# Kernel optimization log

Measured on AMD Instinct MI355X. Metric: run time of the kernel, lower is better.

The kernel has to match this reference:

```python
import jax, jax.numpy as jnp
import numpy as np

B, S_NEW, DIM = 32, 1, 4096
H, KV, HD = 32, 8, 128          # query heads, kv heads, head_dim
PREV = 2048                      # tokens already in the KV cache


def setup_inputs() -> dict:
    key = jax.random.key(0)
    ks = jax.random.split(key, 8)
    return {
        "x": jax.random.normal(ks[0], (B, S_NEW, DIM), jnp.float32),
        "wq": jax.random.normal(ks[1], (DIM, H * HD), jnp.float32) * 0.02,
        "wk": jax.random.normal(ks[2], (DIM, KV * HD), jnp.float32) * 0.02,
        "wv": jax.random.normal(ks[3], (DIM, KV * HD), jnp.float32) * 0.02,
        "wo": jax.random.normal(ks[4], (H * HD, DIM), jnp.float32) * 0.02,
        "cache_k": jax.random.normal(ks[5], (B, PREV, KV, HD), jnp.float32),
        "cache_v": jax.random.normal(ks[6], (B, PREV, KV, HD), jnp.float32),
        "freqs": jax.random.normal(ks[7], (S_NEW, HD // 2), jnp.float32),  # rotary angles (angle of freqs_cis)
    }


def _apply_rope(t, cos, sin):
    # t: [b, s, h, hd]; interleaved pairs as in torch.view_as_complex
    a = t[..., 0::2]
    b = t[..., 1::2]
    c = cos[None, :, None, :]
    s = sin[None, :, None, :]
    ra = a * c - b * s
    rb = a * s + b * c
    return jnp.stack([ra, rb], axis=-1).reshape(t.shape)


def reference(x, wq, wk, wv, wo, cache_k, cache_v, freqs):
    b, s, _ = x.shape  # s == 1 (decode)
    xq = (x @ wq).reshape(b, s, H, HD)
    xk = (x @ wk).reshape(b, s, KV, HD)
    xv = (x @ wv).reshape(b, s, KV, HD)

    cos, sin = jnp.cos(freqs), jnp.sin(freqs)
    xq = _apply_rope(xq, cos, sin)
    xk = _apply_rope(xk, cos, sin)

    # KV-cache append (update_cache_decode)
    k_full = jnp.concatenate([cache_k, xk], axis=1)  # [b, PREV+1, KV, hd]
    v_full = jnp.concatenate([cache_v, xv], axis=1)

    # GQA attention without materializing the expanded cache
    g = H // KV
    q = xq.reshape(b, KV, g, HD)  # s == 1 folded away
    scale = 1.0 / jnp.sqrt(jnp.asarray(HD, x.dtype))
    scores = jnp.einsum("bkgd,bskd->bkgs", q, k_full) * scale  # [b, KV, g, PREV+1]
    attn = jax.nn.softmax(scores, axis=-1)
    out = jnp.einsum("bkgs,bskd->bkgd", attn, v_full)  # [b, KV, g, hd]
    out = out.reshape(b, s, H * HD)
    return out @ wo
```

## Files before the change

kernel.cpp:

```cpp
#include <hip/hip_runtime.h>


#define WS_P1   0
#define WS_QKV  6291456
#define WS_ATTN 6488064
#define WS_P2   6619136

__global__ __launch_bounds__(256) void gemm_skinny(
    const float* __restrict__ X,
    const float* __restrict__ W0, int e0, int ld0,
    const float* __restrict__ W1, int e1, int ld1,
    const float* __restrict__ W2, int ld2,
    float* __restrict__ P, int Ntot)
{
    __shared__ float x_t[128][36];
    __shared__ float2 red[128][33];

    const int nb = blockIdx.x * 256;
    const float* W; int ld, noff;
    if (nb < e0)      { W = W0; ld = ld0; noff = 0;  }
    else if (nb < e1) { W = W1; ld = ld1; noff = e0; }
    else              { W = W2; ld = ld2; noff = e1; }

    const int k0  = blockIdx.y * 128;
    const int tid = threadIdx.x;
    const int cp  = tid & 127;
    const int kg  = tid >> 7;
    const int nn  = nb - noff + cp * 2;

    #pragma unroll
    for (int i = 0; i < 16; ++i) {
        int idx = tid + i * 256;
        int bb = idx >> 7, kk = idx & 127;
        x_t[kk][bb] = X[(size_t)bb * 4096 + k0 + kk];
    }
    __syncthreads();

    float2 acc[32];
    #pragma unroll
    for (int b = 0; b < 32; ++b) { acc[b].x = 0.f; acc[b].y = 0.f; }

    const float* Wp = W + (size_t)k0 * ld + nn;
    for (int kk0 = kg * 64; kk0 < kg * 64 + 64; kk0 += 8) {
        float2 w[8];
        #pragma unroll
        for (int u = 0; u < 8; ++u)
            w[u] = *(const float2*)&Wp[(size_t)(kk0 + u) * ld];
        #pragma unroll
        for (int u = 0; u < 8; ++u) {
            const float* xr = x_t[kk0 + u];
            #pragma unroll
            for (int bq = 0; bq < 8; ++bq) {
                float4 xv = *(const float4*)&xr[bq * 4];
                acc[bq*4+0].x += xv.x * w[u].x; acc[bq*4+0].y += xv.x * w[u].y;
                acc[bq*4+1].x += xv.y * w[u].x; acc[bq*4+1].y += xv.y * w[u].y;
                acc[bq*4+2].x += xv.z * w[u].x; acc[bq*4+2].y += xv.z * w[u].y;
                acc[bq*4+3].x += xv.w * w[u].x; acc[bq*4+3].y += xv.w * w[u].y;
            }
        }
    }

    if (kg == 1) {
        #pragma unroll
        for (int b = 0; b < 32; ++b) red[cp][b] = acc[b];
    }
    __syncthreads();
    if (kg == 0) {
        const int ks = blockIdx.y;
        #pragma unroll
        for (int b = 0; b < 32; ++b) {
            float2 o = red[cp][b];
            float2 v; v.x = acc[b].x + o.x; v.y = acc[b].y + o.y;
            *(float2*)&P[((size_t)ks * 32 + b) * Ntot + nb + cp * 2] = v;
        }
    }
}

__global__ __launch_bounds__(256) void reduce_rope(
    const float* __restrict__ P, const float* __restrict__ freqs,
    float* __restrict__ qkv)
{
    int t = blockIdx.x * 256 + threadIdx.x;
    int b = t / 3072;
    int cp = t - b * 3072;
    int n = cp * 2;
    float sx = 0.f, sy = 0.f;
    #pragma unroll
    for (int ks = 0; ks < 32; ++ks) {
        float2 v = *(const float2*)&P[((size_t)ks * 32 + b) * 6144 + n];
        sx += v.x; sy += v.y;
    }
    if (n < 5120) {
        int d = n & 127;
        float fr = freqs[d >> 1];
        float c = cosf(fr), s = sinf(fr);
        float ra = sx * c - sy * s;
        float rb = sx * s + sy * c;
        if (n < 4096) {
            const float sc = 0.08838834764831845f;
            ra *= sc; rb *= sc;
        }
        sx = ra; sy = rb;
    }
    float2 o; o.x = sx; o.y = sy;
    *(float2*)&qkv[(size_t)b * 6144 + n] = o;
}

__global__ __launch_bounds__(1024) void attn_kernel(
    const float* __restrict__ qkv,
    const float* __restrict__ ck, const float* __restrict__ cv,
    float* __restrict__ ao)
{
    __shared__ float sbuf[8208];
    __shared__ float red[4][4];
    __shared__ float mxv[4];
    __shared__ float inv[4];

    const int b  = blockIdx.x >> 3;
    const int kv = blockIdx.x & 7;
    const int tid = threadIdx.x;
    const int wave = tid >> 6, lane = tid & 63;
    const int psub = (lane >> 4) & 3, dl = lane & 15;

    float q[4][8];
    {
        const float* qb = qkv + (size_t)b * 6144 + kv * 512 + dl * 8;
        #pragma unroll
        for (int h = 0; h < 4; ++h) {
            float4 a = *(const float4*)&qb[h * 128];
            float4 c = *(const float4*)&qb[h * 128 + 4];
            q[h][0]=a.x; q[h][1]=a.y; q[h][2]=a.z; q[h][3]=a.w;
            q[h][4]=c.x; q[h][5]=c.y; q[h][6]=c.z; q[h][7]=c.w;
        }
    }

    if (tid < 16) {
        const float* kr = qkv + (size_t)b * 6144 + 4096 + kv * 128 + dl * 8;
        float4 k0 = *(const float4*)kr;
        float4 k1 = *(const float4*)(kr + 4);
        float p[4];
        #pragma unroll
        for (int h = 0; h < 4; ++h) {
            p[h] = q[h][0]*k0.x + q[h][1]*k0.y + q[h][2]*k0.z + q[h][3]*k0.w
                 + q[h][4]*k1.x + q[h][5]*k1.y + q[h][6]*k1.z + q[h][7]*k1.w;
        }
        #pragma unroll
        for (int off = 1; off < 16; off <<= 1) {
            #pragma unroll
            for (int h = 0; h < 4; ++h) p[h] += __shfl_xor(p[h], off);
        }
        if (dl == 0) {
            #pragma unroll
            for (int h = 0; h < 4; ++h) sbuf[h * 2052 + 2048] = p[h];
        }
    }

    const float* kbase = ck + ((size_t)b * 2048 * 8 + kv) * 128;
    const int srow = wave * 4 + psub;
    for (int it0 = 0; it0 < 32; it0 += 4) {
        float4 kA[4][2];
        #pragma unroll
        for (int u = 0; u < 4; ++u) {
            const float* kr = kbase + (size_t)((it0 + u) * 64 + srow) * 1024 + dl * 8;
            kA[u][0] = *(const float4*)kr;
            kA[u][1] = *(const float4*)(kr + 4);
        }
        #pragma unroll
        for (int u = 0; u < 4; ++u) {
            int s = (it0 + u) * 64 + srow;
            float p[4];
            #pragma unroll
            for (int h = 0; h < 4; ++h) {
                p[h] = q[h][0]*kA[u][0].x + q[h][1]*kA[u][0].y
                     + q[h][2]*kA[u][0].z + q[h][3]*kA[u][0].w
                     + q[h][4]*kA[u][1].x + q[h][5]*kA[u][1].y
                     + q[h][6]*kA[u][1].z + q[h][7]*kA[u][1].w;
            }
            #pragma unroll
            for (int off = 1; off < 16; off <<= 1) {
                #pragma unroll
                for (int h = 0; h < 4; ++h) p[h] += __shfl_xor(p[h], off);
            }
            if (dl == 0) {
                #pragma unroll
                for (int h = 0; h < 4; ++h) sbuf[h * 2052 + s] = p[h];
            }
        }
    }
    __syncthreads();

    const int h = tid >> 8, r = tid & 255;
    float m = -1e30f;
    for (int s = r; s < 2049; s += 256) m = fmaxf(m, sbuf[h * 2052 + s]);
    #pragma unroll
    for (int off = 1; off < 64; off <<= 1) m = fmaxf(m, __shfl_xor(m, off));
    if (lane == 0) red[h][wave & 3] = m;
    __syncthreads();
    if (r == 0)
        mxv[h] = fmaxf(fmaxf(red[h][0], red[h][1]), fmaxf(red[h][2], red[h][3]));
    __syncthreads();
    const float mx = mxv[h];
    float sum = 0.f;
    for (int s = r; s < 2049; s += 256) {
        float p = __expf(sbuf[h * 2052 + s] - mx);
        sbuf[h * 2052 + s] = p;
        sum += p;
    }
    #pragma unroll
    for (int off = 1; off < 64; off <<= 1) sum += __shfl_xor(sum, off);
    if (lane == 0) red[h][wave & 3] = sum;
    __syncthreads();
    if (r == 0) inv[h] = 1.0f / (red[h][0] + red[h][1] + red[h][2] + red[h][3]);
    __syncthreads();

    const int grp = tid >> 5, l32 = tid & 31, d4 = l32 * 4;
    float4 acc[4];
    #pragma unroll
    for (int hh = 0; hh < 4; ++hh) { acc[hh].x=0.f; acc[hh].y=0.f; acc[hh].z=0.f; acc[hh].w=0.f; }
    const float* vbase = cv + ((size_t)b * 2048 * 8 + kv) * 128;
    for (int it = 0; it < 16; ++it) {
        float4 vv[4];
        float pp[4][4];
        #pragma unroll
        for (int j = 0; j < 4; ++j) {
            int s = it * 128 + j * 32 + grp;
            vv[j] = *(const float4*)&vbase[(size_t)s * 1024 + d4];
        }
        #pragma unroll
        for (int j = 0; j < 4; ++j) {
            int s = it * 128 + j * 32 + grp;
            #pragma unroll
            for (int hh = 0; hh < 4; ++hh) pp[j][hh] = sbuf[hh * 2052 + s];
        }
        #pragma unroll
        for (int j = 0; j < 4; ++j) {
            #pragma unroll
            for (int hh = 0; hh < 4; ++hh) {
                acc[hh].x += pp[j][hh] * vv[j].x;
                acc[hh].y += pp[j][hh] * vv[j].y;
                acc[hh].z += pp[j][hh] * vv[j].z;
                acc[hh].w += pp[j][hh] * vv[j].w;
            }
        }
    }
    if (grp == 0) {
        const float* vr = qkv + (size_t)b * 6144 + 5120 + kv * 128;
        float4 v = *(const float4*)&vr[d4];
        #pragma unroll
        for (int hh = 0; hh < 4; ++hh) {
            float p = sbuf[hh * 2052 + 2048];
            acc[hh].x += p * v.x; acc[hh].y += p * v.y;
            acc[hh].z += p * v.z; acc[hh].w += p * v.w;
        }
    }
    __syncthreads();

    #pragma unroll
    for (int hh = 0; hh < 4; ++hh) {
        acc[hh].x += __shfl_down(acc[hh].x, 32);
        acc[hh].y += __shfl_down(acc[hh].y, 32);
        acc[hh].z += __shfl_down(acc[hh].z, 32);
        acc[hh].w += __shfl_down(acc[hh].w, 32);
    }
    if (lane < 32) {
        #pragma unroll
        for (int hh = 0; hh < 4; ++hh)
            *(float4*)&sbuf[wave * 512 + hh * 128 + d4] = acc[hh];
    }
    __syncthreads();

    if (tid < 512) {
        int hh = tid >> 7, d = tid & 127;
        float v = 0.f;
        #pragma unroll
        for (int w = 0; w < 16; ++w) v += sbuf[w * 512 + hh * 128 + d];
        ao[(size_t)b * 4096 + kv * 512 + hh * 128 + d] = v * inv[hh];
    }
}

__global__ __launch_bounds__(256) void reduce_out(
    const float* __restrict__ P, float* __restrict__ out)
{
    int t = blockIdx.x * 256 + threadIdx.x;
    int b = t >> 11;
    int cp = t & 2047;
    int n = cp * 2;
    float sx = 0.f, sy = 0.f;
    #pragma unroll
    for (int ks = 0; ks < 32; ++ks) {
        float2 v = *(const float2*)&P[((size_t)ks * 32 + b) * 4096 + n];
        sx += v.x; sy += v.y;
    }
    float2 o; o.x = sx; o.y = sy;
    *(float2*)&out[(size_t)b * 4096 + n] = o;
}

extern "C" void kernel_launch(void* const* d_in, const int* in_sizes, int n_in,
                              void* d_out, int out_size, void* d_ws, size_t ws_size,
                              hipStream_t stream) {
    const float* x  = (const float*)d_in[0];
    const float* wq = (const float*)d_in[1];
    const float* wk = (const float*)d_in[2];
    const float* wv = (const float*)d_in[3];
    const float* wo = (const float*)d_in[4];
    const float* ck = (const float*)d_in[5];
    const float* cv = (const float*)d_in[6];
    const float* fr = (const float*)d_in[7];
    float* out = (float*)d_out;
    float* ws  = (float*)d_ws;

    float* P1   = ws + WS_P1;
    float* qkv  = ws + WS_QKV;
    float* attn = ws + WS_ATTN;
    float* P2   = ws + WS_P2;

    dim3 g1(24, 32);
    gemm_skinny<<<g1, 256, 0, stream>>>(x, wq, 4096, 4096, wk, 5120, 1024,
                                        wv, 1024, P1, 6144);
    reduce_rope<<<384, 256, 0, stream>>>(P1, fr, qkv);
    attn_kernel<<<256, 1024, 0, stream>>>(qkv, ck, cv, attn);
    dim3 g4(16, 32);
    gemm_skinny<<<g4, 256, 0, stream>>>(attn, wo, 4096, 4096, wo, 4096, 4096,
                                        wo, 4096, P2, 4096);
    reduce_out<<<256, 256, 0, stream>>>(P2, out);
}
```

Baseline: 183.7 us.

## Split attention over sequence chunks with flash-decoding style combine kernel

Replaces the single 1024-thread attention block per (batch, kv-head) with four 256-thread blocks, each covering a 512-token slice of the KV cache. Each block writes its partial max, sum and unnormalized output to a workspace, and a new combine kernel merges them with log-sum-exp rescaling. This raises the block count from 256 to 1024, so more CUs get work and more memory requests are in flight while streaming the cache. The cost is an extra kernel launch and a small workspace round-trip.

```diff
diff --git a/kernel.cpp b/kernel.cpp
--- a/kernel.cpp
+++ b/kernel.cpp
@@ -5,6 +5,7 @@
 #define WS_QKV  6291456
 #define WS_ATTN 6488064
 #define WS_P2   6619136
+#define WS_PA   10813440
 
 __global__ __launch_bounds__(256) void gemm_skinny(
     const float* __restrict__ X,
@@ -106,21 +107,22 @@
     *(float2*)&qkv[(size_t)b * 6144 + n] = o;
 }
 
-__global__ __launch_bounds__(1024) void attn_kernel(
+__global__ __launch_bounds__(256, 4) void attn_split(
     const float* __restrict__ qkv,
     const float* __restrict__ ck, const float* __restrict__ cv,
-    float* __restrict__ ao)
-{
-    __shared__ float sbuf[8208];
-    __shared__ float red[4][4];
-    __shared__ float mxv[4];
-    __shared__ float inv[4];
-
-    const int b  = blockIdx.x >> 3;
-    const int kv = blockIdx.x & 7;
+    float* __restrict__ pa)
+{
+    __shared__ float sbuf[4096];
+    __shared__ float pm[4], pl[4];
+
+    const int blk = blockIdx.x;
+    const int c   = blk & 3;
+    const int kv  = (blk >> 2) & 7;
+    const int b   = blk >> 5;
     const int tid = threadIdx.x;
     const int wave = tid >> 6, lane = tid & 63;
     const int psub = (lane >> 4) & 3, dl = lane & 15;
+    const int s0 = c * 512;
 
     float q[4][8];
     {
@@ -128,13 +130,13 @@
         #pragma unroll
         for (int h = 0; h < 4; ++h) {
             float4 a = *(const float4*)&qb[h * 128];
-            float4 c = *(const float4*)&qb[h * 128 + 4];
+            float4 e = *(const float4*)&qb[h * 128 + 4];
             q[h][0]=a.x; q[h][1]=a.y; q[h][2]=a.z; q[h][3]=a.w;
-            q[h][4]=c.x; q[h][5]=c.y; q[h][6]=c.z; q[h][7]=c.w;
-        }
-    }
-
-    if (tid < 16) {
+            q[h][4]=e.x; q[h][5]=e.y; q[h][6]=e.z; q[h][7]=e.w;
+        }
+    }
+
+    if (c == 3 && tid < 16) {
         const float* kr = qkv + (size_t)b * 6144 + 4096 + kv * 128 + dl * 8;
         float4 k0 = *(const float4*)kr;
         float4 k1 = *(const float4*)(kr + 4);
@@ -151,23 +153,24 @@
         }
         if (dl == 0) {
             #pragma unroll
-            for (int h = 0; h < 4; ++h) sbuf[h * 2052 + 2048] = p[h];
-        }
-    }
-
-    const float* kbase = ck + ((size_t)b * 2048 * 8 + kv) * 128;
+            for (int h = 0; h < 4; ++h) sbuf[h * 520 + 512] = p[h];
+        }
+    }
+
+    const float* kbase = ck + ((size_t)b * 2048 * 8 + kv) * 128
+                            + (size_t)s0 * 1024;
     const int srow = wave * 4 + psub;
     for (int it0 = 0; it0 < 32; it0 += 4) {
         float4 kA[4][2];
         #pragma unroll
         for (int u = 0; u < 4; ++u) {
-            const float* kr = kbase + (size_t)((it0 + u) * 64 + srow) * 1024 + dl * 8;
+            const float* kr = kbase + (size_t)((it0 + u) * 16 + srow) * 1024 + dl * 8;
             kA[u][0] = *(const float4*)kr;
             kA[u][1] = *(const float4*)(kr + 4);
         }
         #pragma unroll
         for (int u = 0; u < 4; ++u) {
-            int s = (it0 + u) * 64 + srow;
+            int s = (it0 + u) * 16 + srow;
             float p[4];
             #pragma unroll
             for (int h = 0; h < 4; ++h) {
@@ -183,54 +186,50 @@
             }
             if (dl == 0) {
                 #pragma unroll
-                for (int h = 0; h < 4; ++h) sbuf[h * 2052 + s] = p[h];
-            }
-        }
-    }
-    __syncthreads();
-
-    const int h = tid >> 8, r = tid & 255;
-    float m = -1e30f;
-    for (int s = r; s < 2049; s += 256) m = fmaxf(m, sbuf[h * 2052 + s]);
-    #pragma unroll
-    for (int off = 1; off < 64; off <<= 1) m = fmaxf(m, __shfl_xor(m, off));
-    if (lane == 0) red[h][wave & 3] = m;
-    __syncthreads();
-    if (r == 0)
-        mxv[h] = fmaxf(fmaxf(red[h][0], red[h][1]), fmaxf(red[h][2], red[h][3]));
-    __syncthreads();
-    const float mx = mxv[h];
-    float sum = 0.f;
-    for (int s = r; s < 2049; s += 256) {
-        float p = __expf(sbuf[h * 2052 + s] - mx);
-        sbuf[h * 2052 + s] = p;
-        sum += p;
-    }
-    #pragma unroll
-    for (int off = 1; off < 64; off <<= 1) sum += __shfl_xor(sum, off);
-    if (lane == 0) red[h][wave & 3] = sum;
-    __syncthreads();
-    if (r == 0) inv[h] = 1.0f / (red[h][0] + red[h][1] + red[h][2] + red[h][3]);
+                for (int h = 0; h < 4; ++h) sbuf[h * 520 + s] = p[h];
+            }
+        }
+    }
+    __syncthreads();
+
+    {
+        const int h = wave;
+        const int nrow = (c == 3) ? 513 : 512;
+        float m = -1e30f;
+        for (int s = lane; s < nrow; s += 64) m = fmaxf(m, sbuf[h * 520 + s]);
+        #pragma unroll
+        for (int off = 1; off < 64; off <<= 1) m = fmaxf(m, __shfl_xor(m, off));
+        float sum = 0.f;
+        for (int s = lane; s < nrow; s += 64) {
+            float p = __expf(sbuf[h * 520 + s] - m);
+            sbuf[h * 520 + s] = p;
+            sum += p;
+        }
+        #pragma unroll
+        for (int off = 1; off < 64; off <<= 1) sum += __shfl_xor(sum, off);
+        if (lane == 0) { pm[h] = m; pl[h] = sum; }
+    }
     __syncthreads();
 
     const int grp = tid >> 5, l32 = tid & 31, d4 = l32 * 4;
     float4 acc[4];
     #pragma unroll
     for (int hh = 0; hh < 4; ++hh) { acc[hh].x=0.f; acc[hh].y=0.f; acc[hh].z=0.f; acc[hh].w=0.f; }
-    const float* vbase = cv + ((size_t)b * 2048 * 8 + kv) * 128;
+    const float* vbase = cv + ((size_t)b * 2048 * 8 + kv) * 128
+                            + (size_t)s0 * 1024;
     for (int it = 0; it < 16; ++it) {
         float4 vv[4];
         float pp[4][4];
         #pragma unroll
         for (int j = 0; j < 4; ++j) {
-            int s = it * 128 + j * 32 + grp;
+            int s = it * 32 + j * 8 + grp;
             vv[j] = *(const float4*)&vbase[(size_t)s * 1024 + d4];
         }
         #pragma unroll
         for (int j = 0; j < 4; ++j) {
-            int s = it * 128 + j * 32 + grp;
-            #pragma unroll
-            for (int hh = 0; hh < 4; ++hh) pp[j][hh] = sbuf[hh * 2052 + s];
+            int s = it * 32 + j * 8 + grp;
+            #pragma unroll
+            for (int hh = 0; hh < 4; ++hh) pp[j][hh] = sbuf[hh * 520 + s];
         }
         #pragma unroll
         for (int j = 0; j < 4; ++j) {
@@ -243,12 +242,12 @@
             }
         }
     }
-    if (grp == 0) {
+    if (c == 3 && grp == 0) {
         const float* vr = qkv + (size_t)b * 6144 + 5120 + kv * 128;
         float4 v = *(const float4*)&vr[d4];
         #pragma unroll
         for (int hh = 0; hh < 4; ++hh) {
-            float p = sbuf[hh * 2052 + 2048];
+            float p = sbuf[hh * 520 + 512];
             acc[hh].x += p * v.x; acc[hh].y += p * v.y;
             acc[hh].z += p * v.z; acc[hh].w += p * v.w;
         }
@@ -256,25 +255,50 @@
     __syncthreads();
 
     #pragma unroll
-    for (int hh = 0; hh < 4; ++hh) {
-        acc[hh].x += __shfl_down(acc[hh].x, 32);
-        acc[hh].y += __shfl_down(acc[hh].y, 32);
-        acc[hh].z += __shfl_down(acc[hh].z, 32);
-        acc[hh].w += __shfl_down(acc[hh].w, 32);
-    }
-    if (lane < 32) {
-        #pragma unroll
-        for (int hh = 0; hh < 4; ++hh)
-            *(float4*)&sbuf[wave * 512 + hh * 128 + d4] = acc[hh];
-    }
-    __syncthreads();
-
-    if (tid < 512) {
-        int hh = tid >> 7, d = tid & 127;
+    for (int hh = 0; hh < 4; ++hh)
+        *(float4*)&sbuf[grp * 512 + hh * 128 + d4] = acc[hh];
+    __syncthreads();
+
+    float* rec = pa + (size_t)blk * 520;
+    for (int t = tid; t < 512; t += 256) {
+        int hh = t >> 7, d = t & 127;
         float v = 0.f;
         #pragma unroll
-        for (int w = 0; w < 16; ++w) v += sbuf[w * 512 + hh * 128 + d];
-        ao[(size_t)b * 4096 + kv * 512 + hh * 128 + d] = v * inv[hh];
+        for (int g = 0; g < 8; ++g) v += sbuf[g * 512 + hh * 128 + d];
+        rec[8 + hh * 128 + d] = v;
+    }
+    if (tid < 4) { rec[tid] = pm[tid]; rec[4 + tid] = pl[tid]; }
+}
+
+__global__ __launch_bounds__(128) void attn_combine(
+    const float* __restrict__ pa, float* __restrict__ ao)
+{
+    __shared__ float w_[4][4];
+    const int g = blockIdx.x;
+    const int d = threadIdx.x;
+    const float* rec = pa + (size_t)g * 4 * 520;
+
+    if (d < 4) {
+        float m0 = rec[0*520 + d], m1 = rec[1*520 + d];
+        float m2 = rec[2*520 + d], m3 = rec[3*520 + d];
+        float M = fmaxf(fmaxf(m0, m1), fmaxf(m2, m3));
+        float e0 = __expf(m0 - M), e1 = __expf(m1 - M);
+        float e2 = __expf(m2 - M), e3 = __expf(m3 - M);
+        float L = rec[0*520 + 4 + d] * e0 + rec[1*520 + 4 + d] * e1
+                + rec[2*520 + 4 + d] * e2 + rec[3*520 + 4 + d] * e3;
+        float inv = 1.0f / L;
+        w_[0][d] = e0 * inv; w_[1][d] = e1 * inv;
+        w_[2][d] = e2 * inv; w_[3][d] = e3 * inv;
+    }
+    __syncthreads();
+
+    #pragma unroll
+    for (int h = 0; h < 4; ++h) {
+        float v = 0.f;
+        #pragma unroll
+        for (int c = 0; c < 4; ++c)
+            v += rec[c*520 + 8 + h*128 + d] * w_[c][h];
+        ao[(size_t)g * 512 + h * 128 + d] = v;
     }
 }
 
@@ -313,12 +337,14 @@
     float* qkv  = ws + WS_QKV;
     float* attn = ws + WS_ATTN;
     float* P2   = ws + WS_P2;
+    float* PA   = ws + WS_PA;
 
     dim3 g1(24, 32);
     gemm_skinny<<<g1, 256, 0, stream>>>(x, wq, 4096, 4096, wk, 5120, 1024,
                                         wv, 1024, P1, 6144);
     reduce_rope<<<384, 256, 0, stream>>>(P1, fr, qkv);
-    attn_kernel<<<256, 1024, 0, stream>>>(qkv, ck, cv, attn);
+    attn_split<<<1024, 256, 0, stream>>>(qkv, ck, cv, PA);
+    attn_combine<<<256, 128, 0, stream>>>(PA, attn);
     dim3 g4(16, 32);
     gemm_skinny<<<g4, 256, 0, stream>>>(attn, wo, 4096, 4096, wo, 4096, 4096,
                                         wo, 4096, P2, 4096);
```

Measured after the change: 183.8 us, median of 2. Within noise of the previous version (+0.1%).
